# Optimization experiments

Hardware: AMD Instinct MI355X
Metric: run time of the kernel (lower is better)

Reference implementation:

```python
import jax, jax.numpy as jnp
import numpy as np


def _prelu(v, a):
    return jnp.where(v >= 0, v, a * v)


def setup_inputs() -> dict:
    key = jax.random.key(0)
    B, H, L, N, DC = 16, 64, 16384, 32, 128
    ks = jax.random.split(key, 10)
    x = jax.random.normal(ks[0], (B, H, L), jnp.float32)
    cond = jax.random.normal(ks[1], (B, DC), jnp.float32)
    # input pointwise linear (applied over channel dim)
    linear_w = jax.random.normal(ks[2], (H, H), jnp.float32) / np.sqrt(H)
    linear_b = jnp.zeros((H,), jnp.float32)
    prelu1_a = jnp.float32(0.25)
    # S4D parameters (S4D-Lin init): A = -exp(log_A_real) + i*A_imag
    log_dt = jax.random.uniform(ks[3], (H,), jnp.float32,
                                minval=float(np.log(1e-3)), maxval=float(np.log(1e-1)))
    log_A_real = jnp.log(0.5 * jnp.ones((H, N), jnp.float32))
    A_imag = jnp.tile(np.pi * jnp.arange(N, dtype=np.float32), (H, 1))
    C_re = 0.5 * jax.random.normal(ks[4], (H, N), jnp.float32)
    C_im = 0.5 * jax.random.normal(ks[5], (H, N), jnp.float32)
    Dskip = jax.random.normal(ks[6], (H,), jnp.float32)
    # S4 output position-wise linear
    out_w = jax.random.normal(ks[7], (H, H), jnp.float32) / np.sqrt(H)
    out_b = jnp.zeros((H,), jnp.float32)
    # FiLM: cond -> (gamma, beta)
    film_w = jax.random.normal(ks[8], (2 * H, DC), jnp.float32) / np.sqrt(DC)
    film_b = jnp.zeros((2 * H,), jnp.float32)
    prelu2_a = jnp.float32(0.25)
    # depthwise 1x1 conv residual: one scalar per channel
    res_w = jax.random.normal(ks[9], (H,), jnp.float32) / np.sqrt(H)
    return dict(x=x, cond=cond, linear_w=linear_w, linear_b=linear_b,
                prelu1_a=prelu1_a, log_dt=log_dt, log_A_real=log_A_real,
                A_imag=A_imag, C_re=C_re, C_im=C_im, Dskip=Dskip,
                out_w=out_w, out_b=out_b, film_w=film_w, film_b=film_b,
                prelu2_a=prelu2_a, res_w=res_w)


def reference(x, cond, linear_w, linear_b, prelu1_a, log_dt, log_A_real,
              A_imag, C_re, C_im, Dskip, out_w, out_b, film_w, film_b,
              prelu2_a, res_w):
    B, H, L = x.shape
    # linear over channel dim (B H L -> B L H -> linear -> B H L)
    h = jnp.einsum('gh,bhl->bgl', linear_w, x) + linear_b[None, :, None]
    h = _prelu(h, prelu1_a)
    # ---- S4D kernel generation (ZOH discretization) ----
    dt = jnp.exp(log_dt)                       # (H,)
    A = -jnp.exp(log_A_real) + 1j * A_imag     # (H, N) complex
    dtA = A * dt[:, None]                      # (H, N)
    Cd = (C_re + 1j * C_im) * (jnp.exp(dtA) - 1.0) / A
    vand = jnp.exp(dtA[:, :, None] * jnp.arange(L, dtype=jnp.float32))  # (H,N,L)
    K = 2.0 * jnp.einsum('hn,hnl->hl', Cd, vand).real  # (H, L)
    # ---- FFT convolution (causal, linear conv via 2L-point FFT) ----
    n = 2 * L
    y = jnp.fft.irfft(jnp.fft.rfft(h, n=n) * jnp.fft.rfft(K, n=n), n=n)[..., :L]
    y = y + h * Dskip[None, :, None]
    # S4 output position-wise linear
    y = jnp.einsum('gh,bhl->bgl', out_w, y) + out_b[None, :, None]
    # BatchNorm1d(affine=False), training-mode batch statistics
    mean = jnp.mean(y, axis=(0, 2), keepdims=True)
    var = jnp.var(y, axis=(0, 2), keepdims=True)
    y = (y - mean) / jnp.sqrt(var + 1e-5)
    # FiLM conditioning
    gb = cond @ film_w.T + film_b              # (B, 2H)
    gamma, beta = jnp.split(gb, 2, axis=-1)
    y = gamma[:, :, None] * y + beta[:, :, None]
    y = _prelu(y, prelu2_a)
    # depthwise 1x1 conv residual
    return y + res_w[None, :, None] * x
```

## Files before the change

kernel.cpp:

```cpp
#include <hip/hip_runtime.h>
#include <math.h>

#define BB 16
#define HH 64
#define LL 16384
#define NST 32
#define LC 256
#define CC 64
#define BL (BB*LL)

typedef _Float16 f16;
typedef f16  f16x8 __attribute__((ext_vector_type(8)));
typedef float f32x4 __attribute__((ext_vector_type(4)));

#define OFF_H   ((size_t)0)
#define OFF_P   ((size_t)8388608)
#define OFF_S   ((size_t)12582912)
#define OFF_T   ((size_t)14680064)
#define OFF_V   ((size_t)16777216)
#define OFF_U   ((size_t)17301504)
#define OFF_PW  ((size_t)17825792)
#define OFF_WL  ((size_t)17833984)
#define OFF_GB  ((size_t)17838080)
#define OFF_BN  ((size_t)17840128)
#define OFF_BNF ((size_t)17840256)

__global__ void k0_setup(const float* __restrict__ log_dt,
                         const float* __restrict__ log_A_real,
                         const float* __restrict__ A_imag,
                         const float* __restrict__ C_re,
                         const float* __restrict__ C_im,
                         const float* __restrict__ cond,
                         const float* __restrict__ film_w,
                         const float* __restrict__ film_b,
                         float* __restrict__ ws) {
    int t = threadIdx.x, bid = blockIdx.x;
    if (bid < 8) {
        float4* pw = (float4*)(ws + OFF_PW);
        float2* wl = (float2*)(ws + OFF_WL);
        int idx = bid * 256 + t;
        int ch = idx >> 5;
        float dt  = expf(log_dt[ch]);
        float are = -expf(log_A_real[idx]);
        float aim = A_imag[idx];
        float dr = are * dt, di = aim * dt;
        float er = expf(dr);
        float wr = er * cosf(di);
        float wi = er * sinf(di);
        float inv = 1.0f / (are * are + aim * aim);
        float gr = ((wr - 1.0f) * are + wi * aim) * inv;
        float gi = (wi * are - (wr - 1.0f) * aim) * inv;
        float cr = C_re[idx], ci = C_im[idx];
        float cdr = cr * gr - ci * gi;
        float cdi = cr * gi + ci * gr;
        pw[idx] = make_float4(wr, wi, 2.0f * cdr, 2.0f * cdi);
        float erL = expf(dr * (float)LC);
        wl[idx] = make_float2(erL * cosf(di * (float)LC), erL * sinf(di * (float)LC));
    } else {
        float* gb = ws + OFF_GB;
        int o = (bid - 8) * 256 + t;
        int b = o >> 7, j = o & 127;
        float acc = film_b[j];
        for (int q = 0; q < 128; q++)
            acc = fmaf(cond[b * 128 + q], film_w[j * 128 + q], acc);
        gb[o] = acc;
    }
}

__global__ __launch_bounds__(256) void kprep(const float* __restrict__ log_dt,
                                             const float* __restrict__ log_A,
                                             const float* __restrict__ A_imag,
                                             const float* __restrict__ Dskip,
                                             float* __restrict__ ws) {
    __shared__ float drs[32], dis[32], c2r[32], c2i[32];
    int ch = blockIdx.x, t = threadIdx.x;
    if (t < 32) {
        float dt = expf(log_dt[ch]);
        float are = -expf(log_A[ch * 32 + t]);
        float aim = A_imag[ch * 32 + t];
        drs[t] = are * dt; dis[t] = aim * dt;
        float4 p = ((const float4*)(ws + OFF_PW))[ch * 32 + t];
        c2r[t] = p.z; c2i[t] = p.w;
    }
    __syncthreads();
    float acc = 0.0f;
    float fd = (float)t;
    for (int n = 0; n < 32; n++) {
        float e = expf(drs[n] * fd);
        float ph = dis[n] * fd;
        acc += c2r[n] * e * cosf(ph) - c2i[n] * e * sinf(ph);
    }
    if (t == 0) acc += Dskip[ch];
    ws[OFF_P + (size_t)ch * 256 + t] = acc;
}

__global__ __launch_bounds__(256) void kbuild(const float* __restrict__ log_dt,
                                              const float* __restrict__ log_A,
                                              const float* __restrict__ A_imag,
                                              float* __restrict__ ws) {
    __shared__ float Kl[256];
    __shared__ float drs[32], dis[32], c2r[32], c2i[32];
    int bid = blockIdx.x;
    int ch = bid >> 4, part = bid & 15;
    int t = threadIdx.x;
    if (t < 32) {
        float dt = expf(log_dt[ch]);
        float are = -expf(log_A[ch * 32 + t]);
        float aim = A_imag[ch * 32 + t];
        drs[t] = are * dt; dis[t] = aim * dt;
        float4 p = ((const float4*)(ws + OFF_PW))[ch * 32 + t];
        c2r[t] = p.z; c2i[t] = p.w;
    }
    Kl[t] = ws[OFF_P + (size_t)ch * 256 + t];
    __syncthreads();
    f16* T = (f16*)(ws + OFF_T) + (size_t)ch * 65536;
    {
        int r0 = part * 16;
#pragma unroll
        for (int i = 0; i < 2; i++) {
            int idx = t + i * 256;
            int row = r0 + (idx >> 5);
            int c0 = (idx & 31) * 8;
            f16 vals[8];
#pragma unroll
            for (int j = 0; j < 8; j++) {
                int c = c0 + j;
                vals[j] = (f16)((c <= row) ? Kl[row - c] : 0.0f);
            }
            *(float4*)(T + (size_t)row * 256 + c0) = *(const float4*)vals;
        }
    }
    if (part < 8) {
        f16* V = (f16*)(ws + OFF_V) + (size_t)ch * 16384;
        int row = part * 8 + (t >> 5);
        int c0 = (t & 31) * 8;
        int n = row & 31;
        f16 vals[8];
#pragma unroll
        for (int j = 0; j < 8; j++) {
            float fe = (float)(255 - (c0 + j));
            float e = expf(drs[n] * fe);
            float ph = dis[n] * fe;
            vals[j] = (f16)((row < 32) ? e * cosf(ph) : e * sinf(ph));
        }
        *(float4*)(V + (size_t)row * 256 + c0) = *(const float4*)vals;
    } else {
        f16* U = (f16*)(ws + OFF_U) + (size_t)ch * 16384;
        int l = (part - 8) * 32 + (t >> 3);
        int c0 = (t & 7) * 8;
        float fl1 = (float)(l + 1);
        f16 vals[8];
#pragma unroll
        for (int nn = 0; nn < 4; nn++) {
            int n = (c0 >> 1) + nn;
            float e = expf(drs[n] * fl1);
            float ph = dis[n] * fl1;
            float wre = e * cosf(ph), wim = e * sinf(ph);
            float re = c2r[n] * wre - c2i[n] * wim;
            float im = c2r[n] * wim + c2i[n] * wre;
            vals[2 * nn]     = (f16)re;
            vals[2 * nn + 1] = (f16)(-im);
        }
        *(float4*)(U + (size_t)l * 64 + c0) = *(const float4*)vals;
    }
}

__global__ __launch_bounds__(256) void k_cm1m(const float* __restrict__ x,
                                              const float* __restrict__ W,
                                              const float* __restrict__ bias,
                                              f16* __restrict__ dst,
                                              const float* __restrict__ aptr) {
    int t = threadIdx.x, bi = blockIdx.x;
    int b = bi >> 6;
    int wv = t >> 6, lane = t & 63;
    int qd = lane >> 4, ln = lane & 15;
    int colw = ((bi & 63) << 8) + wv * 64;
    const float* xb = x + (size_t)b * HH * LL;
    f32x4 acc[4][4];
#pragma unroll
    for (int a = 0; a < 4; a++)
#pragma unroll
        for (int nb = 0; nb < 4; nb++) acc[a][nb] = (f32x4)0.0f;
#pragma unroll
    for (int ks = 0; ks < 2; ks++) {
        f16x8 whi[4], wlo[4];
#pragma unroll
        for (int a = 0; a < 4; a++) {
            const float* wp = W + (size_t)(a * 16 + ln) * 64 + ks * 32 + qd * 8;
#pragma unroll
            for (int j = 0; j < 8; j++) {
                float f = wp[j];
                f16 hv = (f16)f;
                whi[a][j] = hv;
                wlo[a][j] = (f16)(f - (float)hv);
            }
        }
        f16x8 bhi[4], blo[4];
#pragma unroll
        for (int nb = 0; nb < 4; nb++) {
            const float* xp = xb + (size_t)(ks * 32 + qd * 8) * LL + colw + nb * 16 + ln;
#pragma unroll
            for (int j = 0; j < 8; j++) {
                float f = xp[(size_t)j * LL];
                f16 hv = (f16)f;
                bhi[nb][j] = hv;
                blo[nb][j] = (f16)(f - (float)hv);
            }
        }
#pragma unroll
        for (int a = 0; a < 4; a++)
#pragma unroll
            for (int nb = 0; nb < 4; nb++)
                acc[a][nb] = __builtin_amdgcn_mfma_f32_16x16x32_f16(whi[a], bhi[nb], acc[a][nb], 0, 0, 0);
#pragma unroll
        for (int a = 0; a < 4; a++)
#pragma unroll
            for (int nb = 0; nb < 4; nb++)
                acc[a][nb] = __builtin_amdgcn_mfma_f32_16x16x32_f16(whi[a], blo[nb], acc[a][nb], 0, 0, 0);
#pragma unroll
        for (int a = 0; a < 4; a++)
#pragma unroll
            for (int nb = 0; nb < 4; nb++)
                acc[a][nb] = __builtin_amdgcn_mfma_f32_16x16x32_f16(wlo[a], bhi[nb], acc[a][nb], 0, 0, 0);
    }
    float a1 = *aptr;
    f16* dp = dst + (size_t)b * HH * LL;
#pragma unroll
    for (int a = 0; a < 4; a++)
#pragma unroll
        for (int r = 0; r < 4; r++) {
            int g = a * 16 + qd * 4 + r;
            float bb = bias[g];
            f16* gp = dp + (size_t)g * LL + colw + ln;
#pragma unroll
            for (int nb = 0; nb < 4; nb++) {
                float v = acc[a][nb][r] + bb;
                v = (v >= 0.0f) ? v : a1 * v;
                gp[nb * 16] = (f16)v;
            }
        }
}

__global__ __launch_bounds__(256) void k_cm2m(const f16* __restrict__ y1,
                                              const float* __restrict__ W,
                                              const float* __restrict__ bias,
                                              float* __restrict__ dst,
                                              float* __restrict__ ws) {
    __shared__ float bns[64], bnss[64];
    int t = threadIdx.x, bi = blockIdx.x;
    int b = bi >> 6;
    int wv = t >> 6, lane = t & 63;
    int qd = lane >> 4, ln = lane & 15;
    int colw = ((bi & 63) << 8) + wv * 64;
    const f16* yb = y1 + (size_t)b * HH * LL;
    if (t < 64) { bns[t] = 0.0f; bnss[t] = 0.0f; }
    __syncthreads();
    f32x4 acc[4][4];
#pragma unroll
    for (int a = 0; a < 4; a++)
#pragma unroll
        for (int nb = 0; nb < 4; nb++) acc[a][nb] = (f32x4)0.0f;
#pragma unroll
    for (int ks = 0; ks < 2; ks++) {
        f16x8 whi[4], wlo[4];
#pragma unroll
        for (int a = 0; a < 4; a++) {
            const float* wp = W + (size_t)(a * 16 + ln) * 64 + ks * 32 + qd * 8;
#pragma unroll
            for (int j = 0; j < 8; j++) {
                float f = wp[j];
                f16 hv = (f16)f;
                whi[a][j] = hv;
                wlo[a][j] = (f16)(f - (float)hv);
            }
        }
        f16x8 bf[4];
#pragma unroll
        for (int nb = 0; nb < 4; nb++) {
            const f16* yp = yb + (size_t)(ks * 32 + qd * 8) * LL + colw + nb * 16 + ln;
#pragma unroll
            for (int j = 0; j < 8; j++)
                bf[nb][j] = yp[(size_t)j * LL];
        }
#pragma unroll
        for (int a = 0; a < 4; a++)
#pragma unroll
            for (int nb = 0; nb < 4; nb++)
                acc[a][nb] = __builtin_amdgcn_mfma_f32_16x16x32_f16(whi[a], bf[nb], acc[a][nb], 0, 0, 0);
#pragma unroll
        for (int a = 0; a < 4; a++)
#pragma unroll
            for (int nb = 0; nb < 4; nb++)
                acc[a][nb] = __builtin_amdgcn_mfma_f32_16x16x32_f16(wlo[a], bf[nb], acc[a][nb], 0, 0, 0);
    }
    float* dp = dst + (size_t)b * HH * LL;
#pragma unroll
    for (int a = 0; a < 4; a++)
#pragma unroll
        for (int r = 0; r < 4; r++) {
            int g = a * 16 + qd * 4 + r;
            float bb = bias[g];
            float* gp = dp + (size_t)g * LL + colw + ln;
            float s = 0.0f, ssq = 0.0f;
#pragma unroll
            for (int nb = 0; nb < 4; nb++) {
                float v = acc[a][nb][r] + bb;
                gp[nb * 16] = v;
                s += v; ssq += v * v;
            }
#pragma unroll
            for (int off = 1; off < 16; off <<= 1) {
                s += __shfl_xor(s, off);
                ssq += __shfl_xor(ssq, off);
            }
            if (ln == 0) {
                atomicAdd(&bns[g], s);
                atomicAdd(&bnss[g], ssq);
            }
        }
    __syncthreads();
    if (t < 64) {
        float* part = ws + OFF_P;
        part[(size_t)bi * 128 + t] = bns[t];
        part[(size_t)bi * 128 + 64 + t] = bnss[t];
    }
}

__global__ __launch_bounds__(256) void gemmA(float* __restrict__ ws) {
    __shared__ __align__(16) char smem[25600];
    f16* Vs = (f16*)smem;
    f16* Hs = (f16*)(smem + 5120);
    int t = threadIdx.x;
    int bid = blockIdx.x;
    int ch = bid & 63, ntile = bid >> 6;
    const f16* Vm = (const f16*)(ws + OFF_V) + (size_t)ch * 16384;
    const f16* H  = (const f16*)(ws + OFF_H);
    int w = t >> 6, lane = t & 63;
    int qd = lane >> 4, ln = lane & 15;
    f32x4 acc[4][4];
#pragma unroll
    for (int a = 0; a < 4; a++)
#pragma unroll
        for (int nb = 0; nb < 4; nb++) acc[a][nb] = (f32x4)0.0f;
    int colg = ntile * 256 + t;
    const f16* hcol = H + ((size_t)(colg >> 6) * 64 + ch) * 16384 + (size_t)(colg & 63) * 256;
    int vrow = t >> 2, vkg = t & 3;
    for (int k0 = 0; k0 < 256; k0 += 32) {
        __syncthreads();
        *(float4*)&Vs[vrow * 40 + vkg * 8] = *(const float4*)(Vm + vrow * 256 + k0 + vkg * 8);
#pragma unroll
        for (int kg = 0; kg < 4; kg++)
            *(float4*)&Hs[t * 40 + kg * 8] = *(const float4*)(hcol + k0 + kg * 8);
        __syncthreads();
        f16x8 af[4], bf[4];
#pragma unroll
        for (int a = 0; a < 4; a++) af[a] = *(f16x8*)&Vs[(a * 16 + ln) * 40 + qd * 8];
#pragma unroll
        for (int nb = 0; nb < 4; nb++) bf[nb] = *(f16x8*)&Hs[(w * 64 + nb * 16 + ln) * 40 + qd * 8];
#pragma unroll
        for (int a = 0; a < 4; a++)
#pragma unroll
            for (int nb = 0; nb < 4; nb++)
                acc[a][nb] = __builtin_amdgcn_mfma_f32_16x16x32_f16(af[a], bf[nb], acc[a][nb], 0, 0, 0);
    }
    float* P = ws + OFF_P;
#pragma unroll
    for (int a = 0; a < 4; a++)
#pragma unroll
        for (int nb = 0; nb < 4; nb++)
#pragma unroll
            for (int r = 0; r < 4; r++) {
                int row = a * 16 + qd * 4 + r;
                int col = ntile * 256 + w * 64 + nb * 16 + ln;
                P[((size_t)ch * 64 + row) * 1024 + col] = acc[a][nb][r];
            }
}

__global__ __launch_bounds__(256) void k3_scan(float* __restrict__ ws) {
    int tid = blockIdx.x * 256 + threadIdx.x;
    int ch = tid >> 9, b = (tid >> 5) & 15, n = tid & 31;
    const float* P = ws + OFF_P;
    f16* S = (f16*)(ws + OFF_S);
    float2 wl = ((const float2*)(ws + OFF_WL))[ch * 32 + n];
    float sr = 0.0f, si = 0.0f;
    const float* pre = P + ((size_t)ch * 64 + n) * 1024 + b * 64;
    const float* pim = P + ((size_t)ch * 64 + 32 + n) * 1024 + b * 64;
    f16* srow = S + ((size_t)ch * 1024 + b * 64) * 64 + 2 * n;
    for (int c = 0; c < 64; c++) {
        srow[c * 64]     = (f16)sr;
        srow[c * 64 + 1] = (f16)si;
        float pr = pre[c], pi = pim[c];
        float nr = fmaf(wl.x, sr, fmaf(-wl.y, si, pr));
        float ni = fmaf(wl.y, sr, fmaf(wl.x, si, pi));
        sr = nr; si = ni;
    }
}

__global__ __launch_bounds__(256) void gemmMain(float* __restrict__ ws) {
    __shared__ __align__(16) char smem[25600];
    f16* Ts = (f16*)smem;
    f16* Hs = (f16*)(smem + 20480);
    f16* Ys = (f16*)smem;
    int t = threadIdx.x;
    int bid = blockIdx.x;
    int ch = bid & 63, ntile = bid >> 6;
    const f16* Tm = (const f16*)(ws + OFF_T) + (size_t)ch * 65536;
    const f16* Um = (const f16*)(ws + OFF_U) + (size_t)ch * 16384;
    const f16* H  = (const f16*)(ws + OFF_H);
    const f16* St = (const f16*)(ws + OFF_S);
    f16* y1 = (f16*)(ws + OFF_H);
    int w = t >> 6, lane = t & 63;
    int qd = lane >> 4, ln = lane & 15;
    f32x4 acc[4][4];
#pragma unroll
    for (int a = 0; a < 4; a++)
#pragma unroll
        for (int nb = 0; nb < 4; nb++) acc[a][nb] = (f32x4)0.0f;
    int scol = t >> 2, skg = t & 3;
    int colg = ntile * 64 + scol;
    const f16* hcol = H + ((size_t)(colg >> 6) * 64 + ch) * 16384 + (size_t)(colg & 63) * 256;
    const f16* sscol = St + ((size_t)ch * 1024 + colg) * 64;
    for (int k0 = 0; k0 < 256; k0 += 32) {
        __syncthreads();
        if (t >= k0 - 16) {
#pragma unroll
            for (int kg = 0; kg < 4; kg++)
                *(float4*)&Ts[t * 40 + kg * 8] = *(const float4*)(Tm + t * 256 + k0 + kg * 8);
        }
        *(float4*)&Hs[scol * 40 + skg * 8] = *(const float4*)(hcol + k0 + skg * 8);
        __syncthreads();
        if (k0 <= w * 64 + 63) {
            f16x8 bf[4];
#pragma unroll
            for (int nb = 0; nb < 4; nb++) bf[nb] = *(f16x8*)&Hs[(nb * 16 + ln) * 40 + qd * 8];
#pragma unroll
            for (int a = 0; a < 4; a++) {
                if (k0 <= w * 64 + a * 16 + 15) {
                    f16x8 af = *(f16x8*)&Ts[(w * 64 + a * 16 + ln) * 40 + qd * 8];
#pragma unroll
                    for (int nb = 0; nb < 4; nb++)
                        acc[a][nb] = __builtin_amdgcn_mfma_f32_16x16x32_f16(af, bf[nb], acc[a][nb], 0, 0, 0);
                }
            }
        }
    }
    for (int k0 = 0; k0 < 64; k0 += 32) {
        __syncthreads();
#pragma unroll
        for (int kg = 0; kg < 4; kg++)
            *(float4*)&Ts[t * 40 + kg * 8] = *(const float4*)(Um + t * 64 + k0 + kg * 8);
        *(float4*)&Hs[scol * 40 + skg * 8] = *(const float4*)(sscol + k0 + skg * 8);
        __syncthreads();
        f16x8 bf[4];
#pragma unroll
        for (int nb = 0; nb < 4; nb++) bf[nb] = *(f16x8*)&Hs[(nb * 16 + ln) * 40 + qd * 8];
#pragma unroll
        for (int a = 0; a < 4; a++) {
            f16x8 af = *(f16x8*)&Ts[(w * 64 + a * 16 + ln) * 40 + qd * 8];
#pragma unroll
            for (int nb = 0; nb < 4; nb++)
                acc[a][nb] = __builtin_amdgcn_mfma_f32_16x16x32_f16(af, bf[nb], acc[a][nb], 0, 0, 0);
        }
    }
    int ocol = t >> 2, ojg = t & 3;
    int ocolg = ntile * 64 + ocol;
    f16* ybase = y1 + ((size_t)(ocolg >> 6) * 64 + ch) * 16384 + (size_t)(ocolg & 63) * 256;
    for (int hf = 0; hf < 2; hf++) {
        __syncthreads();
        if ((w >> 1) == hf) {
            int jl0 = (w & 1) * 64;
#pragma unroll
            for (int a = 0; a < 4; a++)
#pragma unroll
                for (int nb = 0; nb < 4; nb++)
#pragma unroll
                    for (int r = 0; r < 4; r++)
                        Ys[(nb * 16 + ln) * 136 + jl0 + a * 16 + qd * 4 + r] = (f16)acc[a][nb][r];
        }
        __syncthreads();
#pragma unroll
        for (int i = 0; i < 4; i++)
            *(float4*)(ybase + hf * 128 + ojg * 32 + i * 8) =
                *(const float4*)&Ys[ocol * 136 + ojg * 32 + i * 8];
    }
}

__global__ __launch_bounds__(256) void k5c_bnfin(float* __restrict__ ws) {
    int ch = blockIdx.x;
    int t = threadIdx.x;
    const float* part = ws + OFF_P;
    float s = 0.0f, ss = 0.0f;
#pragma unroll
    for (int i = 0; i < 4; i++) {
        int pb = t + i * 256;
        s  += part[(size_t)pb * 128 + ch];
        ss += part[(size_t)pb * 128 + 64 + ch];
    }
    for (int off = 32; off; off >>= 1) {
        s += __shfl_xor(s, off);
        ss += __shfl_xor(ss, off);
    }
    __shared__ float as_[4], ass_[4];
    int wv = t >> 6;
    if ((t & 63) == 0) { as_[wv] = s; ass_[wv] = ss; }
    __syncthreads();
    if (t == 0) {
        float S = as_[0] + as_[1] + as_[2] + as_[3];
        float SS = ass_[0] + ass_[1] + ass_[2] + ass_[3];
        float cnt = (float)BL;
        float mean = S / cnt;
        float var = SS / cnt - mean * mean;
        ws[OFF_BNF + ch] = mean;
        ws[OFF_BNF + 64 + ch] = 1.0f / sqrtf(var + 1e-5f);
    }
}

__global__ __launch_bounds__(256) void k6_final(const float* __restrict__ x,
                                                const float* __restrict__ ws,
                                                const float* __restrict__ a2p,
                                                const float* __restrict__ res_w,
                                                float* __restrict__ out) {
    int bi = blockIdx.x;
    int t = threadIdx.x;
    int row = bi >> 4;
    int b = row >> 6, ch = row & 63;
    float gamma = ws[OFF_GB + b * 128 + ch];
    float beta  = ws[OFF_GB + b * 128 + 64 + ch];
    float mean = ws[OFF_BNF + ch];
    float inv  = ws[OFF_BNF + 64 + ch];
    float scale = gamma * inv;
    float shift = beta - scale * mean;
    float rw = res_w[ch];
    float a2 = *a2p;
    size_t i4 = (size_t)row * (LL / 4) + (size_t)(bi & 15) * 256 + t;
    float4 y = ((const float4*)out)[i4];
    float4 xv = ((const float4*)x)[i4];
    float v;
    v = fmaf(scale, y.x, shift); v = (v >= 0.0f) ? v : a2 * v; y.x = fmaf(rw, xv.x, v);
    v = fmaf(scale, y.y, shift); v = (v >= 0.0f) ? v : a2 * v; y.y = fmaf(rw, xv.y, v);
    v = fmaf(scale, y.z, shift); v = (v >= 0.0f) ? v : a2 * v; y.z = fmaf(rw, xv.z, v);
    v = fmaf(scale, y.w, shift); v = (v >= 0.0f) ? v : a2 * v; y.w = fmaf(rw, xv.w, v);
    ((float4*)out)[i4] = y;
}

extern "C" void kernel_launch(void* const* d_in, const int* in_sizes, int n_in,
                              void* d_out, int out_size, void* d_ws, size_t ws_size,
                              hipStream_t stream) {
    const float* x        = (const float*)d_in[0];
    const float* cond     = (const float*)d_in[1];
    const float* linear_w = (const float*)d_in[2];
    const float* linear_b = (const float*)d_in[3];
    const float* prelu1_a = (const float*)d_in[4];
    const float* log_dt   = (const float*)d_in[5];
    const float* log_A    = (const float*)d_in[6];
    const float* A_imag   = (const float*)d_in[7];
    const float* C_re     = (const float*)d_in[8];
    const float* C_im     = (const float*)d_in[9];
    const float* Dskip    = (const float*)d_in[10];
    const float* out_w    = (const float*)d_in[11];
    const float* out_b    = (const float*)d_in[12];
    const float* film_w   = (const float*)d_in[13];
    const float* film_b   = (const float*)d_in[14];
    const float* prelu2_a = (const float*)d_in[15];
    const float* res_w    = (const float*)d_in[16];
    float* ws  = (float*)d_ws;
    float* out = (float*)d_out;
    f16* hbuf = (f16*)(ws + OFF_H);
    f16* y1   = (f16*)(ws + OFF_H);

    hipLaunchKernelGGL(k0_setup, dim3(16), dim3(256), 0, stream,
                       log_dt, log_A, A_imag, C_re, C_im, cond, film_w, film_b, ws);
    hipLaunchKernelGGL(kprep, dim3(64), dim3(256), 0, stream,
                       log_dt, log_A, A_imag, Dskip, ws);
    hipLaunchKernelGGL(kbuild, dim3(1024), dim3(256), 0, stream,
                       log_dt, log_A, A_imag, ws);
    hipLaunchKernelGGL(k_cm1m, dim3(1024), dim3(256), 0, stream,
                       x, linear_w, linear_b, hbuf, prelu1_a);
    hipLaunchKernelGGL(gemmA, dim3(256), dim3(256), 0, stream, ws);
    hipLaunchKernelGGL(k3_scan, dim3(128), dim3(256), 0, stream, ws);
    hipLaunchKernelGGL(gemmMain, dim3(1024), dim3(256), 0, stream, ws);
    hipLaunchKernelGGL(k_cm2m, dim3(1024), dim3(256), 0, stream,
                       y1, out_w, out_b, out, ws);
    hipLaunchKernelGGL(k5c_bnfin, dim3(64), dim3(256), 0, stream, ws);
    hipLaunchKernelGGL(k6_final, dim3(16384), dim3(256), 0, stream,
                       x, ws, prelu2_a, res_w, out);
}
```

Measured before the change: 288.3 us.

## Recompute output projection in final kernel instead of storing fp32 intermediate

The stats pass now only accumulates BatchNorm sums and no longer writes the fp32 projected activations. The final kernel recomputes the output pointwise linear with MFMA from the f16 buffer and fuses normalization, FiLM, PReLU and the residual. This removes a large fp32 write and read-back of the intermediate. In exchange it runs the GEMM twice and uses a less vectorized store pattern in the final kernel.

```diff
diff --git a/kernel.cpp b/kernel.cpp
--- a/kernel.cpp
+++ b/kernel.cpp
@@ -241,10 +241,9 @@
         }
 }
 
-__global__ __launch_bounds__(256) void k_cm2m(const f16* __restrict__ y1,
+__global__ __launch_bounds__(256) void k_cm2s(const f16* __restrict__ y1,
                                               const float* __restrict__ W,
                                               const float* __restrict__ bias,
-                                              float* __restrict__ dst,
                                               float* __restrict__ ws) {
     __shared__ float bns[64], bnss[64];
     int t = threadIdx.x, bi = blockIdx.x;
@@ -293,19 +292,16 @@
             for (int nb = 0; nb < 4; nb++)
                 acc[a][nb] = __builtin_amdgcn_mfma_f32_16x16x32_f16(wlo[a], bf[nb], acc[a][nb], 0, 0, 0);
     }
-    float* dp = dst + (size_t)b * HH * LL;
 #pragma unroll
     for (int a = 0; a < 4; a++)
 #pragma unroll
         for (int r = 0; r < 4; r++) {
             int g = a * 16 + qd * 4 + r;
             float bb = bias[g];
-            float* gp = dp + (size_t)g * LL + colw + ln;
             float s = 0.0f, ssq = 0.0f;
 #pragma unroll
             for (int nb = 0; nb < 4; nb++) {
                 float v = acc[a][nb][r] + bb;
-                gp[nb * 16] = v;
                 s += v; ssq += v * v;
             }
 #pragma unroll
@@ -515,32 +511,84 @@
     }
 }
 
-__global__ __launch_bounds__(256) void k6_final(const float* __restrict__ x,
-                                                const float* __restrict__ ws,
-                                                const float* __restrict__ a2p,
-                                                const float* __restrict__ res_w,
-                                                float* __restrict__ out) {
-    int bi = blockIdx.x;
-    int t = threadIdx.x;
-    int row = bi >> 4;
-    int b = row >> 6, ch = row & 63;
-    float gamma = ws[OFF_GB + b * 128 + ch];
-    float beta  = ws[OFF_GB + b * 128 + 64 + ch];
-    float mean = ws[OFF_BNF + ch];
-    float inv  = ws[OFF_BNF + 64 + ch];
-    float scale = gamma * inv;
-    float shift = beta - scale * mean;
-    float rw = res_w[ch];
+__global__ __launch_bounds__(256) void k6m(const f16* __restrict__ y1,
+                                           const float* __restrict__ W,
+                                           const float* __restrict__ bias,
+                                           const float* __restrict__ x,
+                                           const float* __restrict__ ws,
+                                           const float* __restrict__ a2p,
+                                           const float* __restrict__ res_w,
+                                           float* __restrict__ out) {
+    int t = threadIdx.x, bi = blockIdx.x;
+    int b = bi >> 6;
+    int wv = t >> 6, lane = t & 63;
+    int qd = lane >> 4, ln = lane & 15;
+    int colw = ((bi & 63) << 8) + wv * 64;
+    const f16* yb = y1 + (size_t)b * HH * LL;
+    f32x4 acc[4][4];
+#pragma unroll
+    for (int a = 0; a < 4; a++)
+#pragma unroll
+        for (int nb = 0; nb < 4; nb++) acc[a][nb] = (f32x4)0.0f;
+#pragma unroll
+    for (int ks = 0; ks < 2; ks++) {
+        f16x8 whi[4], wlo[4];
+#pragma unroll
+        for (int a = 0; a < 4; a++) {
+            const float* wp = W + (size_t)(a * 16 + ln) * 64 + ks * 32 + qd * 8;
+#pragma unroll
+            for (int j = 0; j < 8; j++) {
+                float f = wp[j];
+                f16 hv = (f16)f;
+                whi[a][j] = hv;
+                wlo[a][j] = (f16)(f - (float)hv);
+            }
+        }
+        f16x8 bf[4];
+#pragma unroll
+        for (int nb = 0; nb < 4; nb++) {
+            const f16* yp = yb + (size_t)(ks * 32 + qd * 8) * LL + colw + nb * 16 + ln;
+#pragma unroll
+            for (int j = 0; j < 8; j++)
+                bf[nb][j] = yp[(size_t)j * LL];
+        }
+#pragma unroll
+        for (int a = 0; a < 4; a++)
+#pragma unroll
+            for (int nb = 0; nb < 4; nb++)
+                acc[a][nb] = __builtin_amdgcn_mfma_f32_16x16x32_f16(whi[a], bf[nb], acc[a][nb], 0, 0, 0);
+#pragma unroll
+        for (int a = 0; a < 4; a++)
+#pragma unroll
+            for (int nb = 0; nb < 4; nb++)
+                acc[a][nb] = __builtin_amdgcn_mfma_f32_16x16x32_f16(wlo[a], bf[nb], acc[a][nb], 0, 0, 0);
+    }
     float a2 = *a2p;
-    size_t i4 = (size_t)row * (LL / 4) + (size_t)(bi & 15) * 256 + t;
-    float4 y = ((const float4*)out)[i4];
-    float4 xv = ((const float4*)x)[i4];
-    float v;
-    v = fmaf(scale, y.x, shift); v = (v >= 0.0f) ? v : a2 * v; y.x = fmaf(rw, xv.x, v);
-    v = fmaf(scale, y.y, shift); v = (v >= 0.0f) ? v : a2 * v; y.y = fmaf(rw, xv.y, v);
-    v = fmaf(scale, y.z, shift); v = (v >= 0.0f) ? v : a2 * v; y.z = fmaf(rw, xv.z, v);
-    v = fmaf(scale, y.w, shift); v = (v >= 0.0f) ? v : a2 * v; y.w = fmaf(rw, xv.w, v);
-    ((float4*)out)[i4] = y;
+    const float* xb = x + (size_t)b * HH * LL;
+    float* ob = out + (size_t)b * HH * LL;
+#pragma unroll
+    for (int a = 0; a < 4; a++)
+#pragma unroll
+        for (int r = 0; r < 4; r++) {
+            int g = a * 16 + qd * 4 + r;
+            float bb = bias[g];
+            float gamma = ws[OFF_GB + b * 128 + g];
+            float beta  = ws[OFF_GB + b * 128 + 64 + g];
+            float mean = ws[OFF_BNF + g];
+            float inv  = ws[OFF_BNF + 64 + g];
+            float scale = gamma * inv;
+            float shift = beta - scale * mean;
+            float rw = res_w[g];
+            const float* xp = xb + (size_t)g * LL + colw + ln;
+            float* op = ob + (size_t)g * LL + colw + ln;
+#pragma unroll
+            for (int nb = 0; nb < 4; nb++) {
+                float v = acc[a][nb][r] + bb;
+                v = fmaf(scale, v, shift);
+                v = (v >= 0.0f) ? v : a2 * v;
+                op[nb * 16] = fmaf(rw, xp[nb * 16], v);
+            }
+        }
 }
 
 extern "C" void kernel_launch(void* const* d_in, const int* in_sizes, int n_in,
@@ -579,9 +627,9 @@
     hipLaunchKernelGGL(gemmA, dim3(256), dim3(256), 0, stream, ws);
     hipLaunchKernelGGL(k3_scan, dim3(128), dim3(256), 0, stream, ws);
     hipLaunchKernelGGL(gemmMain, dim3(1024), dim3(256), 0, stream, ws);
-    hipLaunchKernelGGL(k_cm2m, dim3(1024), dim3(256), 0, stream,
-                       y1, out_w, out_b, out, ws);
+    hipLaunchKernelGGL(k_cm2s, dim3(1024), dim3(256), 0, stream,
+                       y1, out_w, out_b, ws);
     hipLaunchKernelGGL(k5c_bnfin, dim3(64), dim3(256), 0, stream, ws);
-    hipLaunchKernelGGL(k6_final, dim3(16384), dim3(256), 0, stream,
-                       x, ws, prelu2_a, res_w, out);
-}
+    hipLaunchKernelGGL(k6m, dim3(1024), dim3(256), 0, stream,
+                       y1, out_w, out_b, x, ws, prelu2_a, res_w, out);
+}
```

Measured after the change: 283.2 us. About the same (-1.8%).
